# Kernel optimization log

Hardware: AMD Instinct MI355X
Metric: run time of the kernel (lower is better)

## Reference

```python
import jax, jax.numpy as jnp
import numpy as np
import math

MAXL = 3
TAUS = [16, 16, 16, 16]
OUT_TAUS = [16, 16, 16, 16]
BM_CNT = 1.0
BM_EPS = 1e-5

# (l1, l2, l) triples in the kernel's triple-loop order, bucketed by output l
TRIPLES = {l: [] for l in range(MAXL + 1)}
for _l1 in range(MAXL + 1):
    for _l2 in range(_l1 + 1):
        for _l in range(_l1 - _l2, min(_l1 + _l2, MAXL) + 1):
            TRIPLES[_l].append((_l1, _l2))

MIDDLE_TAUS = [sum(TAUS[a] * TAUS[b] for (a, b) in TRIPLES[l]) for l in range(MAXL + 1)]


def _cg_coef(l1, m1, l2, m2, l, m):
    if m1 + m2 != m:
        return 0.0
    f = math.factorial
    pre = math.sqrt((2 * l + 1) * f(l1 + l2 - l) * f(l1 - l2 + l) * f(-l1 + l2 + l) / f(l1 + l2 + l + 1))
    pre *= math.sqrt(f(l + m) * f(l - m) * f(l1 - m1) * f(l1 + m1) * f(l2 - m2) * f(l2 + m2))
    s = 0.0
    for k in range(0, l1 + l2 - l + 1):
        d = [k, l1 + l2 - l - k, l1 - m1 - k, l2 + m2 - k, l - l2 + m1 + k, l - l1 - m2 + k]
        if any(x < 0 for x in d):
            continue
        den = 1.0
        for x in d:
            den *= f(x)
        s += (-1.0) ** k / den
    return pre * s


def _cg_tensor(l1, l2, l):
    t = np.zeros((2 * l1 + 1, 2 * l2 + 1, 2 * l + 1), dtype=np.float32)
    for i, m1 in enumerate(range(-l1, l1 + 1)):
        for j, m2 in enumerate(range(-l2, l2 + 1)):
            m = m1 + m2
            if -l <= m <= l:
                t[i, j, m + l] = _cg_coef(l1, m1, l2, m2, l, m)
    return t

CG = {}
for _l in range(MAXL + 1):
    for (_l1, _l2) in TRIPLES[_l]:
        CG[(_l1, _l2, _l)] = jnp.asarray(_cg_tensor(_l1, _l2, _l))

# complex-multiply contraction tensor: (a*b)[k] = a[i] b[j] CM[i,j,k]
_CM = np.zeros((2, 2, 2), dtype=np.float32)
_CM[0, 0, 0] = 1.0; _CM[1, 1, 0] = -1.0; _CM[0, 1, 1] = 1.0; _CM[1, 0, 1] = 1.0
CM = jnp.asarray(_CM)


def setup_inputs() -> dict:
    key = jax.random.key(0)
    k1, k2, k3 = jax.random.split(key, 3)
    in_len = sum(TAUS[l] * (2 * l + 1) for l in range(MAXL + 1))  # 256
    wlen = sum(OUT_TAUS[l] * MIDDLE_TAUS[l] for l in range(MAXL + 1))  # 90112
    activations = jax.random.normal(k1, (2048, in_len, 2), dtype=jnp.float32)
    W = 0.05 * jax.random.uniform(k2, (wlen, 2), dtype=jnp.float32)
    bn_stds = jax.random.uniform(k3, (sum(MIDDLE_TAUS),), dtype=jnp.float32)
    return {"activations": activations, "W": W, "bn_stds": bn_stds}


def reference(activations, W, bn_stds):
    B = activations.shape[0]
    # split input into per-l parts: [B, tau_l, 2l+1, 2]
    Fs = []
    st = 0
    for l in range(MAXL + 1):
        ln = TAUS[l] * (2 * l + 1)
        Fs.append(activations[:, st:st + ln, :].reshape(B, TAUS[l], 2 * l + 1, 2))
        st += ln
    outs = []
    w_st = 0
    s_st = 0
    for l in range(MAXL + 1):
        # Clebsch-Gordan products feeding output degree l
        mids = []
        for (l1, l2) in TRIPLES[l]:
            c = jnp.einsum('btmi,bsnj,mnp,ijk->btspk', Fs[l1], Fs[l2], CG[(l1, l2, l)], CM)
            mids.append(c.reshape(B, TAUS[l1] * TAUS[l2], 2 * l + 1, 2))
        mid = jnp.concatenate(mids, axis=1)  # [B, M_l, 2l+1, 2]
        Ml = MIDDLE_TAUS[l]
        # fused batchnorm: per-middle-channel std over batch and m, moving average update
        batch_std = jnp.sqrt(jnp.mean(jnp.sum(mid * mid, axis=-1), axis=(0, 2)))  # [M_l]
        mov = bn_stds[s_st:s_st + Ml]
        new_std = (mov * BM_CNT + batch_std) / (BM_CNT + 1.0)
        mid = mid / (new_std + BM_EPS)[None, :, None, None]
        # complex linear mix over middle channels -> out_taus[l]
        wl = jax.lax.dynamic_slice_in_dim(W, w_st, OUT_TAUS[l] * Ml, axis=0).reshape(OUT_TAUS[l], Ml, 2)
        out_l = jnp.einsum('oci,bcmj,ijk->bomk', wl, mid, CM)
        outs.append(out_l.reshape(B, OUT_TAUS[l] * (2 * l + 1), 2))
        w_st += OUT_TAUS[l] * Ml
        s_st += Ml
    return jnp.concatenate(outs, axis=1)  # [B, 256, 2]
```

## Files before the change

kernel.cpp:

```cpp
#include <hip/hip_runtime.h>
#include <math.h>

typedef __attribute__((ext_vector_type(8))) short bf16x8;
typedef __attribute__((ext_vector_type(4))) float f32x4;

constexpr double cfact(int n){ double r=1.0; for(int i=2;i<=n;++i) r*=(double)i; return r; }
constexpr double csqrt_(double x){ double g=(x>1.0)?x:1.0; for(int i=0;i<100;++i) g=0.5*(g+x/g); return g; }
constexpr double cg_coef_(int l1,int m1,int l2,int m2,int l,int m){
  double pre = csqrt_((double)(2*l+1)*cfact(l1+l2-l)*cfact(l1-l2+l)*cfact(-l1+l2+l)/cfact(l1+l2+l+1));
  pre = pre*csqrt_(cfact(l+m)*cfact(l-m)*cfact(l1-m1)*cfact(l1+m1)*cfact(l2-m2)*cfact(l2+m2));
  double s=0.0;
  for(int k=0;k<=l1+l2-l;++k){
    int d0=k,d1=l1+l2-l-k,d2=l1-m1-k,d3=l2+m2-k,d4=l-l2+m1+k,d5=l-l1-m2+k;
    if(d0<0||d1<0||d2<0||d3<0||d4<0||d5<0) continue;
    double den=cfact(d0)*cfact(d1)*cfact(d2)*cfact(d3)*cfact(d4)*cfact(d5);
    s+=((k&1)?-1.0:1.0)/den;
  }
  return pre*s;
}
struct CGList{ int n; float coef[64]; int mi[64]; int ni[64]; int pi[64]; };
constexpr CGList build_cg(int l1,int l2,int l){
  CGList T{};
  for(int i=0;i<2*l1+1;++i){
    for(int j=0;j<2*l2+1;++j){
      int m1=i-l1, m2=j-l2, m=m1+m2;
      if(m<-l||m>l) continue;
      double c=cg_coef_(l1,m1,l2,m2,l,m);
      if(c>1e-12||c<-1e-12){
        T.coef[T.n]=(float)c; T.mi[T.n]=i; T.ni[T.n]=j; T.pi[T.n]=m+l; T.n++;
      }
    }
  }
  return T;
}

__device__ __host__ constexpr int AOFF(int l){ return l==0?0: l==1?16: l==2?64:144; }
__device__ __host__ constexpr int MLs(int l){ return l==0?1024: l==1?1536: l==2?1792:1536; }
__device__ __host__ constexpr int WOFF(int l){ return l==0?0: l==1?16384: l==2?40960:69632; }
__device__ __host__ constexpr int SOFF(int l){ return l==0?0: l==1?1024: l==2?2560:4352; }
__device__ __host__ constexpr int NTRI(int l){ return l==0?4: l==1?6: l==2?7:6; }
__device__ __host__ constexpr int ABASE(int l){ return l==0?0: l==1?65536: l==2?163840:278528; }
__device__ __host__ constexpr size_t MBW(int l){ return l==0?0 : l==1?2097152 : l==2?11534336 : 29884416; }
#define MID_OFF 1048576
#define MID_BYTES ((size_t)51904512*4)

#define DEVFN __device__ __forceinline__
#define LPITCH 144
#define APITCH 132

DEVFN unsigned f2bf2(float x, float y){
  unsigned ux = __float_as_uint(x); ux = (ux + 0x7FFFu + ((ux>>16)&1u)) >> 16;
  unsigned uy = __float_as_uint(y); uy = (uy + 0x7FFFu + ((uy>>16)&1u)) >> 16;
  return (ux & 0xFFFFu) | (uy << 16);
}

template<int L1,int L2,int L>
DEVFN void cg_accum(const float2* F1, const float2* F2, float2* mid){
  constexpr CGList T = build_cg(L1,L2,L);
  #pragma unroll
  for(int e=0;e<T.n;++e){
    const float c = T.coef[e];
    const float2 a = F1[T.mi[e]];
    const float2 b = F2[T.ni[e]];
    float pr = a.x*b.x - a.y*b.y;
    float pim= a.x*b.y + a.y*b.x;
    mid[T.pi[e]].x += c*pr;
    mid[T.pi[e]].y += c*pim;
  }
}

template<int L1,int L2,int L,int Q>
DEVFN void k1_body(const float2* __restrict__ acts, int b0, int u, int bh,
                   float& ssa, float& ssb, unsigned* __restrict__ midw){
  constexpr int N1=2*L1+1, N2=2*L2+1, NP=2*L+1, Ml=MLs(L);
  const int t = u>>3, s0 = (u&7)*2;
  unsigned* midq = midw ? (midw + MBW(L) + (size_t)Q*256) : nullptr;
  #pragma unroll 2
  for(int bi=0;bi<8;++bi){
    const int row = bh*8 + bi;
    const float2* arow = acts + row*256;
    float2 F1[N1], F2a[N2], F2b[N2], mida[NP], midb[NP];
    #pragma unroll
    for(int m=0;m<N1;++m) F1[m]=arow[AOFF(L1)+t*N1+m];
    #pragma unroll
    for(int n=0;n<N2;++n){
      F2a[n]=arow[AOFF(L2)+s0*N2+n];
      F2b[n]=arow[AOFF(L2)+(s0+1)*N2+n];
    }
    #pragma unroll
    for(int p=0;p<NP;++p){ mida[p]=make_float2(0.f,0.f); midb[p]=make_float2(0.f,0.f); }
    cg_accum<L1,L2,L>(F1,F2a,mida);
    cg_accum<L1,L2,L>(F1,F2b,midb);
    #pragma unroll
    for(int p=0;p<NP;++p){
      ssa += mida[p].x*mida[p].x + mida[p].y*mida[p].y;
      ssb += midb[p].x*midb[p].x + midb[p].y*midb[p].y;
    }
    if(midq){
      const size_t nrow = (size_t)(b0+row)*NP;
      #pragma unroll
      for(int p=0;p<NP;++p){
        uint2 v; v.x = f2bf2(mida[p].x, mida[p].y); v.y = f2bf2(midb[p].x, midb[p].y);
        ((uint2*)(midq + (nrow+p)*Ml))[u] = v;
      }
    }
  }
}

__global__ __launch_bounds__(256) void k_sumsq(const float* __restrict__ act,
                                               float* __restrict__ sumsq,
                                               unsigned* __restrict__ midw){
  __shared__ float2 acts[16*256];
  int bid=blockIdx.x;
  const int order[23] = {22,16,21,18,15,20,13,9,14,8,17,7,12,6,10,3,5,19,2,11,1,4,0};
  int ti = order[bid>>7];
  int b0 = (bid&127)*16;
  const int tid = threadIdx.x;
  {
    const float4* ag = (const float4*)act + (size_t)b0*128;
    float4* as4 = (float4*)acts;
    #pragma unroll
    for(int j=0;j<8;++j) as4[j*256+tid] = ag[j*256+tid];
  }
  __syncthreads();
  const int u = tid & 127, bh = tid >> 7;
  float ssa=0.f, ssb=0.f;
  switch(ti){
    case 0:  k1_body<0,0,0,0>(acts,b0,u,bh,ssa,ssb,midw); break;
    case 1:  k1_body<1,1,0,1>(acts,b0,u,bh,ssa,ssb,midw); break;
    case 2:  k1_body<2,2,0,2>(acts,b0,u,bh,ssa,ssb,midw); break;
    case 3:  k1_body<3,3,0,3>(acts,b0,u,bh,ssa,ssb,midw); break;
    case 4:  k1_body<1,0,1,0>(acts,b0,u,bh,ssa,ssb,midw); break;
    case 5:  k1_body<1,1,1,1>(acts,b0,u,bh,ssa,ssb,midw); break;
    case 6:  k1_body<2,1,1,2>(acts,b0,u,bh,ssa,ssb,midw); break;
    case 7:  k1_body<2,2,1,3>(acts,b0,u,bh,ssa,ssb,midw); break;
    case 8:  k1_body<3,2,1,4>(acts,b0,u,bh,ssa,ssb,midw); break;
    case 9:  k1_body<3,3,1,5>(acts,b0,u,bh,ssa,ssb,midw); break;
    case 10: k1_body<1,1,2,0>(acts,b0,u,bh,ssa,ssb,midw); break;
    case 11: k1_body<2,0,2,1>(acts,b0,u,bh,ssa,ssb,midw); break;
    case 12: k1_body<2,1,2,2>(acts,b0,u,bh,ssa,ssb,midw); break;
    case 13: k1_body<2,2,2,3>(acts,b0,u,bh,ssa,ssb,midw); break;
    case 14: k1_body<3,1,2,4>(acts,b0,u,bh,ssa,ssb,midw); break;
    case 15: k1_body<3,2,2,5>(acts,b0,u,bh,ssa,ssb,midw); break;
    case 16: k1_body<3,3,2,6>(acts,b0,u,bh,ssa,ssb,midw); break;
    case 17: k1_body<2,1,3,0>(acts,b0,u,bh,ssa,ssb,midw); break;
    case 18: k1_body<2,2,3,1>(acts,b0,u,bh,ssa,ssb,midw); break;
    case 19: k1_body<3,0,3,2>(acts,b0,u,bh,ssa,ssb,midw); break;
    case 20: k1_body<3,1,3,3>(acts,b0,u,bh,ssa,ssb,midw); break;
    case 21: k1_body<3,2,3,4>(acts,b0,u,bh,ssa,ssb,midw); break;
    default: k1_body<3,3,3,5>(acts,b0,u,bh,ssa,ssb,midw); break;
  }
  atomicAdd(&sumsq[ti*256 + 2*u],     ssa);
  atomicAdd(&sumsq[ti*256 + 2*u + 1], ssb);
}

__global__ __launch_bounds__(256) void k_buildA(const float* __restrict__ W,
                                                const float* __restrict__ bn,
                                                const float* __restrict__ sumsq,
                                                short* __restrict__ A){
  int idx = blockIdx.x*256 + threadIdx.x;
  if(idx>=5888) return;
  int l = (idx<1024)?0 : (idx<2560)?1 : (idx<4352)?2 : 3;
  float divi = (l==0)?(1.f/2048.f) : (l==1)?(1.f/6144.f) : (l==2)?(1.f/10240.f) : (1.f/14336.f);
  float bstd = sqrtf(sumsq[idx]*divi);
  float nstd = 0.5f*(bn[idx]+bstd);
  float s = 1.f/(nstd+1e-5f);
  int c = idx - SOFF(l);
  int Ml = MLs(l);
  const float2* wbase = (const float2*)W + WOFF(l) + c;
  unsigned* Aw = (unsigned*)(A + ABASE(l));
  for(int o=0;o<16;++o){
    float2 w = wbase[(size_t)o*Ml];
    Aw[(size_t)o*Ml + c]      = f2bf2(w.x*s, -w.y*s);
    Aw[(size_t)(o+16)*Ml + c] = f2bf2(w.y*s,  w.x*s);
  }
}

template<int L>
DEVFN void k4_panel(int tg, const unsigned* __restrict__ midl,
                    const short* __restrict__ A_l, float* __restrict__ out,
                    unsigned* ldsA){
  constexpr int NP = 2*L+1;
  constexpr int Ml = MLs(L);
  constexpr int NK = Ml/16;
  constexpr int P  = NK/8;
  const int tid = threadIdx.x;
  const int lane = tid & 63, w = tid >> 6;
  const int col = lane & 15, quad = lane >> 4;
  const int nt = tg*8 + w;
  const unsigned* Aw = (const unsigned*)A_l;
  const unsigned* bp = midl + (size_t)(nt*16 + col)*Ml + quad*4;

  const int r0 = tid >> 5,        j0 = (tid & 31)*4;
  const int r1 = (tid+512) >> 5,  j1 = j0;

  f32x4 cR = {0.f,0.f,0.f,0.f};
  f32x4 cI = {0.f,0.f,0.f,0.f};
  {
    uint4 v0 = *(const uint4*)(Aw + (size_t)r0*Ml + j0);
    uint4 v1 = *(const uint4*)(Aw + (size_t)r1*Ml + j1);
    *(uint4*)(ldsA + r0*APITCH + j0) = v0;
    *(uint4*)(ldsA + r1*APITCH + j1) = v1;
  }
  __syncthreads();
  for(int p=0; p<P; ++p){
    const unsigned* buf  = ldsA + (p&1)*(32*APITCH);
    unsigned* nbuf = ldsA + ((p+1)&1)*(32*APITCH);
    uint4 v0, v1;
    if(p+1 < P){
      v0 = *(const uint4*)(Aw + (size_t)r0*Ml + (p+1)*128 + j0);
      v1 = *(const uint4*)(Aw + (size_t)r1*Ml + (p+1)*128 + j1);
    }
    const unsigned* bpp = bp + p*128;
    const unsigned* a0 = buf + col*APITCH + quad*4;
    const unsigned* a1 = buf + (col+16)*APITCH + quad*4;
    #pragma unroll
    for(int c=0; c<8; ++c){
      bf16x8 b  = *(const bf16x8*)(bpp + c*16);
      bf16x8 A0 = *(const bf16x8*)(a0 + c*16);
      bf16x8 A1 = *(const bf16x8*)(a1 + c*16);
      cR = __builtin_amdgcn_mfma_f32_16x16x32_bf16(A0, b, cR, 0, 0, 0);
      cI = __builtin_amdgcn_mfma_f32_16x16x32_bf16(A1, b, cI, 0, 0, 0);
    }
    if(p+1 < P){
      *(uint4*)(nbuf + r0*APITCH + j0) = v0;
      *(uint4*)(nbuf + r1*APITCH + j1) = v1;
    }
    __syncthreads();
  }
  const int n = nt*16 + col;
  const int b = n / NP, pp = n % NP;
  float2* out2 = (float2*)out;
  #pragma unroll
  for(int i=0;i<4;++i){
    const int o = quad*4 + i;
    out2[(size_t)b*256 + AOFF(L) + o*NP + pp] = make_float2(cR[i], cI[i]);
  }
}

__global__ __launch_bounds__(512) void k_gemm4(const unsigned* __restrict__ midw,
                                               const short* __restrict__ A,
                                               float* __restrict__ out){
  __shared__ unsigned ldsA[2*32*APITCH];
  const int bid = blockIdx.x;
  if(bid < 16)       k4_panel<0>(bid,       midw+MBW(0), A+ABASE(0), out, ldsA);
  else if(bid < 64)  k4_panel<1>(bid - 16,  midw+MBW(1), A+ABASE(1), out, ldsA);
  else if(bid < 144) k4_panel<2>(bid - 64,  midw+MBW(2), A+ABASE(2), out, ldsA);
  else               k4_panel<3>(bid - 144, midw+MBW(3), A+ABASE(3), out, ldsA);
}

template<int L1,int L2,int L>
DEVFN void phase1(const float2* __restrict__ act2, unsigned* ldsw,
                  int half, int c0, int bh4, int b_lo, int b_hi, int n0){
  constexpr int N1=2*L1+1, N2=2*L2+1, NP=2*L+1;
  const int s  = c0 & 15;
  const int t1 = half*8 + (c0>>4);
  const int t2 = t1 + 4;
  for(int b = b_lo + bh4; b <= b_hi; b += 4){
    const float2* arow = act2 + (size_t)b*256;
    float2 F1a[N1], F1b[N1], F2[N2], mida[NP], midb[NP];
    #pragma unroll
    for(int m=0;m<N1;++m){
      F1a[m]=arow[AOFF(L1)+t1*N1+m];
      F1b[m]=arow[AOFF(L1)+t2*N1+m];
    }
    #pragma unroll
    for(int n=0;n<N2;++n) F2[n]=arow[AOFF(L2)+s*N2+n];
    #pragma unroll
    for(int p=0;p<NP;++p){ mida[p]=make_float2(0.f,0.f); midb[p]=make_float2(0.f,0.f); }
    cg_accum<L1,L2,L>(F1a,F2,mida);
    cg_accum<L1,L2,L>(F1b,F2,midb);
    int nb = b*NP - n0;
    #pragma unroll
    for(int p=0;p<NP;++p){
      int n = nb + p;
      if(n>=0 && n<32){
        ldsw[n*LPITCH + c0]      = f2bf2(mida[p].x, mida[p].y);
        ldsw[n*LPITCH + c0 + 64] = f2bf2(midb[p].x, midb[p].y);
      }
    }
  }
}

template<int L>
DEVFN void p1_dispatch(int q, int half, const float2* __restrict__ act2, unsigned* ldsw,
                       int c0,int bh4,int b_lo,int b_hi,int n0){
  if constexpr(L==0){
    switch(q){
      case 0: phase1<0,0,0>(act2,ldsw,half,c0,bh4,b_lo,b_hi,n0); break;
      case 1: phase1<1,1,0>(act2,ldsw,half,c0,bh4,b_lo,b_hi,n0); break;
      case 2: phase1<2,2,0>(act2,ldsw,half,c0,bh4,b_lo,b_hi,n0); break;
      default:phase1<3,3,0>(act2,ldsw,half,c0,bh4,b_lo,b_hi,n0); break;
    }
  } else if constexpr(L==1){
    switch(q){
      case 0: phase1<1,0,1>(act2,ldsw,half,c0,bh4,b_lo,b_hi,n0); break;
      case 1: phase1<1,1,1>(act2,ldsw,half,c0,bh4,b_lo,b_hi,n0); break;
      case 2: phase1<2,1,1>(act2,ldsw,half,c0,bh4,b_lo,b_hi,n0); break;
      case 3: phase1<2,2,1>(act2,ldsw,half,c0,bh4,b_lo,b_hi,n0); break;
      case 4: phase1<3,2,1>(act2,ldsw,half,c0,bh4,b_lo,b_hi,n0); break;
      default:phase1<3,3,1>(act2,ldsw,half,c0,bh4,b_lo,b_hi,n0); break;
    }
  } else if constexpr(L==2){
    switch(q){
      case 0: phase1<1,1,2>(act2,ldsw,half,c0,bh4,b_lo,b_hi,n0); break;
      case 1: phase1<2,0,2>(act2,ldsw,half,c0,bh4,b_lo,b_hi,n0); break;
      case 2: phase1<2,1,2>(act2,ldsw,half,c0,bh4,b_lo,b_hi,n0); break;
      case 3: phase1<2,2,2>(act2,ldsw,half,c0,bh4,b_lo,b_hi,n0); break;
      case 4: phase1<3,1,2>(act2,ldsw,half,c0,bh4,b_lo,b_hi,n0); break;
      case 5: phase1<3,2,2>(act2,ldsw,half,c0,bh4,b_lo,b_hi,n0); break;
      default:phase1<3,3,2>(act2,ldsw,half,c0,bh4,b_lo,b_hi,n0); break;
    }
  } else {
    switch(q){
      case 0: phase1<2,1,3>(act2,ldsw,half,c0,bh4,b_lo,b_hi,n0); break;
      case 1: phase1<2,2,3>(act2,ldsw,half,c0,bh4,b_lo,b_hi,n0); break;
      case 2: phase1<3,0,3>(act2,ldsw,half,c0,bh4,b_lo,b_hi,n0); break;
      case 3: phase1<3,1,3>(act2,ldsw,half,c0,bh4,b_lo,b_hi,n0); break;
      case 4: phase1<3,2,3>(act2,ldsw,half,c0,bh4,b_lo,b_hi,n0); break;
      default:phase1<3,3,3>(act2,ldsw,half,c0,bh4,b_lo,b_hi,n0); break;
    }
  }
}

template<int L>
DEVFN void k3_gemm(int n0, const float2* __restrict__ act2,
                   const short* __restrict__ A_l, float* __restrict__ out,
                   unsigned* lds){
  constexpr int NP = 2*L+1;
  constexpr int NT = NTRI(L);
  constexpr int pitchA = 2*MLs(L);
  const int tid = threadIdx.x;
  const int lane = tid & 63, wsub = tid >> 6;
  const int col = lane & 15, quad = lane >> 4;
  const int nh = wsub & 1, mh = wsub >> 1;
  const int c0 = tid & 63, bh4 = tid >> 6;
  const int b_lo = n0 / NP;
  const int b_hi = (n0 + 31) / NP;

  f32x4 acc = {0.f,0.f,0.f,0.f};
  const short* Ar = A_l + (size_t)(col + mh*16) * pitchA + quad*8;
  const int lds_rd = (nh*16 + col)*LPITCH + quad*4;

  for(int chunk = 0; chunk < 2*NT; ++chunk){
    const int q = chunk >> 1, half = chunk & 1;
    unsigned* buf = lds + (chunk & 1)*(32*LPITCH);
    p1_dispatch<L>(q, half, act2, buf, c0, bh4, b_lo, b_hi, n0);
    __syncthreads();
    const int kbase = q*512 + half*256;
    const char* ldsb = (const char*)(buf + lds_rd);
    #pragma unroll
    for(int ks=0; ks<8; ++ks){
      bf16x8 a = *(const bf16x8*)(Ar + kbase + ks*32);
      bf16x8 b = *(const bf16x8*)(ldsb + ks*64);
      acc = __builtin_amdgcn_mfma_f32_16x16x32_bf16(a, b, acc, 0, 0, 0);
    }
  }
  const int n = n0 + nh*16 + col;
  const int b = n / NP, p = n % NP;
  #pragma unroll
  for(int i=0;i<4;++i){
    const int o = quad*4 + i;
    out[((size_t)b*256 + AOFF(L) + o*NP + p)*2 + mh] = acc[i];
  }
}

__global__ __launch_bounds__(256) void k_gemm(const float* __restrict__ act,
                                              const short* __restrict__ A,
                                              float* __restrict__ out){
  __shared__ unsigned lds[2*32*LPITCH];
  const int bid = blockIdx.x;
  const float2* act2 = (const float2*)act;
  if(bid < 64)       k3_gemm<0>((bid      )*32, act2, A + ABASE(0), out, lds);
  else if(bid < 256) k3_gemm<1>((bid - 64 )*32, act2, A + ABASE(1), out, lds);
  else if(bid < 576) k3_gemm<2>((bid - 256)*32, act2, A + ABASE(2), out, lds);
  else               k3_gemm<3>((bid - 576)*32, act2, A + ABASE(3), out, lds);
}

extern "C" void kernel_launch(void* const* d_in, const int* in_sizes, int n_in,
                              void* d_out, int out_size, void* d_ws, size_t ws_size,
                              hipStream_t stream) {
  const float* act = (const float*)d_in[0];
  const float* W   = (const float*)d_in[1];
  const float* bn  = (const float*)d_in[2];
  float* out = (float*)d_out;

  float* sumsq = (float*)d_ws;
  short* A     = (short*)((char*)d_ws + 24576);
  const size_t REQ = (size_t)MID_OFF + MID_BYTES;
  unsigned* midw = (ws_size >= REQ) ? (unsigned*)((char*)d_ws + MID_OFF) : nullptr;

  hipMemsetAsync(sumsq, 0, 5888*sizeof(float), stream);
  hipLaunchKernelGGL(k_sumsq,  dim3(23*128), dim3(256), 0, stream, act, sumsq, midw);
  hipLaunchKernelGGL(k_buildA, dim3(23),     dim3(256), 0, stream, W, bn, sumsq, A);
  if(midw)
    hipLaunchKernelGGL(k_gemm4, dim3(256),  dim3(512), 0, stream, (const unsigned*)midw, A, out);
  else
    hipLaunchKernelGGL(k_gemm,  dim3(1024), dim3(256), 0, stream, act, A, out);
}
```

Baseline: 171.2 us.

## Fuse CG product recomputation into GEMM and drop materialized middle buffer

Before, k_sumsq wrote the full bf16 middle tensor to workspace and k_gemm4 streamed it back as GEMM operand. Now each block takes one (triple, 8-batch) tile, stages activations in LDS, recomputes the CG products into an LDS bf16 tile, runs the MFMA against the weight slice, and atomically adds partial outputs per triple into a zeroed output. This removes the large global write and reread of the middle tensor. The cost is recomputing the CG products, extra atomics, an output memset, and poor MFMA use for small-l tiles where many waves sit idle.

```diff
diff --git a/kernel.cpp b/kernel.cpp
--- a/kernel.cpp
+++ b/kernel.cpp
@@ -38,15 +38,10 @@
 __device__ __host__ constexpr int MLs(int l){ return l==0?1024: l==1?1536: l==2?1792:1536; }
 __device__ __host__ constexpr int WOFF(int l){ return l==0?0: l==1?16384: l==2?40960:69632; }
 __device__ __host__ constexpr int SOFF(int l){ return l==0?0: l==1?1024: l==2?2560:4352; }
-__device__ __host__ constexpr int NTRI(int l){ return l==0?4: l==1?6: l==2?7:6; }
 __device__ __host__ constexpr int ABASE(int l){ return l==0?0: l==1?65536: l==2?163840:278528; }
 __device__ __host__ constexpr size_t MBW(int l){ return l==0?0 : l==1?2097152 : l==2?11534336 : 29884416; }
-#define MID_OFF 1048576
-#define MID_BYTES ((size_t)51904512*4)
 
 #define DEVFN __device__ __forceinline__
-#define LPITCH 144
-#define APITCH 132
 
 DEVFN unsigned f2bf2(float x, float y){
   unsigned ux = __float_as_uint(x); ux = (ux + 0x7FFFu + ((ux>>16)&1u)) >> 16;
@@ -176,205 +171,124 @@
   }
 }
 
-template<int L>
-DEVFN void k4_panel(int tg, const unsigned* __restrict__ midl,
-                    const short* __restrict__ A_l, float* __restrict__ out,
-                    unsigned* ldsA){
-  constexpr int NP = 2*L+1;
+template<int L1,int L2,int L,int Q>
+DEVFN void kf_body(const float* __restrict__ act, const short* __restrict__ A_l,
+                   float* __restrict__ out, int b0, char* smem){
+  constexpr int N1=2*L1+1, N2=2*L2+1, NP=2*L+1;
   constexpr int Ml = MLs(L);
-  constexpr int NK = Ml/16;
-  constexpr int P  = NK/8;
+  constexpr int S1 = 16*N1;
+  constexpr int SH = (L1==L2)?0:S1;
+  constexpr int S12 = S1 + ((L1==L2)?0:16*N2);
+  constexpr int F4B = S12/2;
+  constexpr int ROWS = 8*NP;
+  constexpr int NTIL = (ROWS+15)/16;
+  constexpr int BP = 68;
   const int tid = threadIdx.x;
+  float2* sa = (float2*)smem;
+  unsigned* btile = (unsigned*)(smem + (size_t)8*S12*sizeof(float2));
+  {
+    const float4* actg = (const float4*)act;
+    float4* s4 = (float4*)smem;
+    for(int i=tid; i<8*F4B; i+=256){
+      int lb = i / F4B, e = i - lb*F4B;
+      int so = (e < S1/2) ? (AOFF(L1)/2 + e) : (AOFF(L2)/2 + (e - S1/2));
+      s4[i] = actg[(size_t)(b0+lb)*128 + so];
+    }
+  }
+  __syncthreads();
   const int lane = tid & 63, w = tid >> 6;
   const int col = lane & 15, quad = lane >> 4;
-  const int nt = tg*8 + w;
+  const int up = tid & 31, bi = tid >> 5;
   const unsigned* Aw = (const unsigned*)A_l;
-  const unsigned* bp = midl + (size_t)(nt*16 + col)*Ml + quad*4;
-
-  const int r0 = tid >> 5,        j0 = (tid & 31)*4;
-  const int r1 = (tid+512) >> 5,  j1 = j0;
-
   f32x4 cR = {0.f,0.f,0.f,0.f};
   f32x4 cI = {0.f,0.f,0.f,0.f};
-  {
-    uint4 v0 = *(const uint4*)(Aw + (size_t)r0*Ml + j0);
-    uint4 v1 = *(const uint4*)(Aw + (size_t)r1*Ml + j1);
-    *(uint4*)(ldsA + r0*APITCH + j0) = v0;
-    *(uint4*)(ldsA + r1*APITCH + j1) = v1;
-  }
-  __syncthreads();
-  for(int p=0; p<P; ++p){
-    const unsigned* buf  = ldsA + (p&1)*(32*APITCH);
-    unsigned* nbuf = ldsA + ((p+1)&1)*(32*APITCH);
-    uint4 v0, v1;
-    if(p+1 < P){
-      v0 = *(const uint4*)(Aw + (size_t)r0*Ml + (p+1)*128 + j0);
-      v1 = *(const uint4*)(Aw + (size_t)r1*Ml + (p+1)*128 + j1);
-    }
-    const unsigned* bpp = bp + p*128;
-    const unsigned* a0 = buf + col*APITCH + quad*4;
-    const unsigned* a1 = buf + (col+16)*APITCH + quad*4;
-    #pragma unroll
-    for(int c=0; c<8; ++c){
-      bf16x8 b  = *(const bf16x8*)(bpp + c*16);
-      bf16x8 A0 = *(const bf16x8*)(a0 + c*16);
-      bf16x8 A1 = *(const bf16x8*)(a1 + c*16);
-      cR = __builtin_amdgcn_mfma_f32_16x16x32_bf16(A0, b, cR, 0, 0, 0);
-      cI = __builtin_amdgcn_mfma_f32_16x16x32_bf16(A1, b, cI, 0, 0, 0);
-    }
-    if(p+1 < P){
-      *(uint4*)(nbuf + r0*APITCH + j0) = v0;
-      *(uint4*)(nbuf + r1*APITCH + j1) = v1;
+  #pragma unroll
+  for(int cc=0; cc<4; ++cc){
+    {
+      const int u = cc*32 + up;
+      const int t = u>>3, s0 = (u&7)*2;
+      const float2* f1b = sa + bi*S12 + t*N1;
+      const float2* f2b = sa + bi*S12 + SH;
+      float2 F1[N1], F2a[N2], F2b[N2], mida[NP], midb[NP];
+      #pragma unroll
+      for(int m=0;m<N1;++m) F1[m]=f1b[m];
+      #pragma unroll
+      for(int n=0;n<N2;++n){ F2a[n]=f2b[s0*N2+n]; F2b[n]=f2b[(s0+1)*N2+n]; }
+      #pragma unroll
+      for(int p=0;p<NP;++p){ mida[p]=make_float2(0.f,0.f); midb[p]=make_float2(0.f,0.f); }
+      cg_accum<L1,L2,L>(F1,F2a,mida);
+      cg_accum<L1,L2,L>(F1,F2b,midb);
+      unsigned* bw = btile + 2*up;
+      #pragma unroll
+      for(int p=0;p<NP;++p){
+        const int r = bi*NP + p;
+        bw[r*BP]   = f2bf2(mida[p].x, mida[p].y);
+        bw[r*BP+1] = f2bf2(midb[p].x, midb[p].y);
+      }
     }
     __syncthreads();
-  }
-  const int n = nt*16 + col;
-  const int b = n / NP, pp = n % NP;
-  float2* out2 = (float2*)out;
-  #pragma unroll
-  for(int i=0;i<4;++i){
-    const int o = quad*4 + i;
-    out2[(size_t)b*256 + AOFF(L) + o*NP + pp] = make_float2(cR[i], cI[i]);
-  }
-}
-
-__global__ __launch_bounds__(512) void k_gemm4(const unsigned* __restrict__ midw,
+    if(w < NTIL){
+      const unsigned* Ab = Aw + Q*256 + cc*64 + quad*4;
+      const unsigned* bb = btile + (w*16+col)*BP + quad*4;
+      #pragma unroll
+      for(int ks=0; ks<4; ++ks){
+        bf16x8 A0 = *(const bf16x8*)(Ab + (size_t)col*Ml + ks*16);
+        bf16x8 A1 = *(const bf16x8*)(Ab + (size_t)(col+16)*Ml + ks*16);
+        bf16x8 b  = *(const bf16x8*)(bb + ks*16);
+        cR = __builtin_amdgcn_mfma_f32_16x16x32_bf16(A0, b, cR, 0, 0, 0);
+        cI = __builtin_amdgcn_mfma_f32_16x16x32_bf16(A1, b, cI, 0, 0, 0);
+      }
+    }
+    __syncthreads();
+  }
+  if(w < NTIL){
+    const int r = w*16 + col;
+    if(r < ROWS){
+      const int b = b0 + r/NP, p = r - (r/NP)*NP;
+      float* ob = out + ((size_t)b*256 + AOFF(L) + p)*2;
+      #pragma unroll
+      for(int i=0;i<4;++i){
+        const int o = quad*4 + i;
+        atomicAdd(ob + o*NP*2,     cR[i]);
+        atomicAdd(ob + o*NP*2 + 1, cI[i]);
+      }
+    }
+  }
+}
+
+__global__ __launch_bounds__(256) void k_fused(const float* __restrict__ act,
                                                const short* __restrict__ A,
                                                float* __restrict__ out){
-  __shared__ unsigned ldsA[2*32*APITCH];
+  __shared__ __align__(16) char smem[29696];
   const int bid = blockIdx.x;
-  if(bid < 16)       k4_panel<0>(bid,       midw+MBW(0), A+ABASE(0), out, ldsA);
-  else if(bid < 64)  k4_panel<1>(bid - 16,  midw+MBW(1), A+ABASE(1), out, ldsA);
-  else if(bid < 144) k4_panel<2>(bid - 64,  midw+MBW(2), A+ABASE(2), out, ldsA);
-  else               k4_panel<3>(bid - 144, midw+MBW(3), A+ABASE(3), out, ldsA);
-}
-
-template<int L1,int L2,int L>
-DEVFN void phase1(const float2* __restrict__ act2, unsigned* ldsw,
-                  int half, int c0, int bh4, int b_lo, int b_hi, int n0){
-  constexpr int N1=2*L1+1, N2=2*L2+1, NP=2*L+1;
-  const int s  = c0 & 15;
-  const int t1 = half*8 + (c0>>4);
-  const int t2 = t1 + 4;
-  for(int b = b_lo + bh4; b <= b_hi; b += 4){
-    const float2* arow = act2 + (size_t)b*256;
-    float2 F1a[N1], F1b[N1], F2[N2], mida[NP], midb[NP];
-    #pragma unroll
-    for(int m=0;m<N1;++m){
-      F1a[m]=arow[AOFF(L1)+t1*N1+m];
-      F1b[m]=arow[AOFF(L1)+t2*N1+m];
-    }
-    #pragma unroll
-    for(int n=0;n<N2;++n) F2[n]=arow[AOFF(L2)+s*N2+n];
-    #pragma unroll
-    for(int p=0;p<NP;++p){ mida[p]=make_float2(0.f,0.f); midb[p]=make_float2(0.f,0.f); }
-    cg_accum<L1,L2,L>(F1a,F2,mida);
-    cg_accum<L1,L2,L>(F1b,F2,midb);
-    int nb = b*NP - n0;
-    #pragma unroll
-    for(int p=0;p<NP;++p){
-      int n = nb + p;
-      if(n>=0 && n<32){
-        ldsw[n*LPITCH + c0]      = f2bf2(mida[p].x, mida[p].y);
-        ldsw[n*LPITCH + c0 + 64] = f2bf2(midb[p].x, midb[p].y);
-      }
-    }
-  }
-}
-
-template<int L>
-DEVFN void p1_dispatch(int q, int half, const float2* __restrict__ act2, unsigned* ldsw,
-                       int c0,int bh4,int b_lo,int b_hi,int n0){
-  if constexpr(L==0){
-    switch(q){
-      case 0: phase1<0,0,0>(act2,ldsw,half,c0,bh4,b_lo,b_hi,n0); break;
-      case 1: phase1<1,1,0>(act2,ldsw,half,c0,bh4,b_lo,b_hi,n0); break;
-      case 2: phase1<2,2,0>(act2,ldsw,half,c0,bh4,b_lo,b_hi,n0); break;
-      default:phase1<3,3,0>(act2,ldsw,half,c0,bh4,b_lo,b_hi,n0); break;
-    }
-  } else if constexpr(L==1){
-    switch(q){
-      case 0: phase1<1,0,1>(act2,ldsw,half,c0,bh4,b_lo,b_hi,n0); break;
-      case 1: phase1<1,1,1>(act2,ldsw,half,c0,bh4,b_lo,b_hi,n0); break;
-      case 2: phase1<2,1,1>(act2,ldsw,half,c0,bh4,b_lo,b_hi,n0); break;
-      case 3: phase1<2,2,1>(act2,ldsw,half,c0,bh4,b_lo,b_hi,n0); break;
-      case 4: phase1<3,2,1>(act2,ldsw,half,c0,bh4,b_lo,b_hi,n0); break;
-      default:phase1<3,3,1>(act2,ldsw,half,c0,bh4,b_lo,b_hi,n0); break;
-    }
-  } else if constexpr(L==2){
-    switch(q){
-      case 0: phase1<1,1,2>(act2,ldsw,half,c0,bh4,b_lo,b_hi,n0); break;
-      case 1: phase1<2,0,2>(act2,ldsw,half,c0,bh4,b_lo,b_hi,n0); break;
-      case 2: phase1<2,1,2>(act2,ldsw,half,c0,bh4,b_lo,b_hi,n0); break;
-      case 3: phase1<2,2,2>(act2,ldsw,half,c0,bh4,b_lo,b_hi,n0); break;
-      case 4: phase1<3,1,2>(act2,ldsw,half,c0,bh4,b_lo,b_hi,n0); break;
-      case 5: phase1<3,2,2>(act2,ldsw,half,c0,bh4,b_lo,b_hi,n0); break;
-      default:phase1<3,3,2>(act2,ldsw,half,c0,bh4,b_lo,b_hi,n0); break;
-    }
-  } else {
-    switch(q){
-      case 0: phase1<2,1,3>(act2,ldsw,half,c0,bh4,b_lo,b_hi,n0); break;
-      case 1: phase1<2,2,3>(act2,ldsw,half,c0,bh4,b_lo,b_hi,n0); break;
-      case 2: phase1<3,0,3>(act2,ldsw,half,c0,bh4,b_lo,b_hi,n0); break;
-      case 3: phase1<3,1,3>(act2,ldsw,half,c0,bh4,b_lo,b_hi,n0); break;
-      case 4: phase1<3,2,3>(act2,ldsw,half,c0,bh4,b_lo,b_hi,n0); break;
-      default:phase1<3,3,3>(act2,ldsw,half,c0,bh4,b_lo,b_hi,n0); break;
-    }
-  }
-}
-
-template<int L>
-DEVFN void k3_gemm(int n0, const float2* __restrict__ act2,
-                   const short* __restrict__ A_l, float* __restrict__ out,
-                   unsigned* lds){
-  constexpr int NP = 2*L+1;
-  constexpr int NT = NTRI(L);
-  constexpr int pitchA = 2*MLs(L);
-  const int tid = threadIdx.x;
-  const int lane = tid & 63, wsub = tid >> 6;
-  const int col = lane & 15, quad = lane >> 4;
-  const int nh = wsub & 1, mh = wsub >> 1;
-  const int c0 = tid & 63, bh4 = tid >> 6;
-  const int b_lo = n0 / NP;
-  const int b_hi = (n0 + 31) / NP;
-
-  f32x4 acc = {0.f,0.f,0.f,0.f};
-  const short* Ar = A_l + (size_t)(col + mh*16) * pitchA + quad*8;
-  const int lds_rd = (nh*16 + col)*LPITCH + quad*4;
-
-  for(int chunk = 0; chunk < 2*NT; ++chunk){
-    const int q = chunk >> 1, half = chunk & 1;
-    unsigned* buf = lds + (chunk & 1)*(32*LPITCH);
-    p1_dispatch<L>(q, half, act2, buf, c0, bh4, b_lo, b_hi, n0);
-    __syncthreads();
-    const int kbase = q*512 + half*256;
-    const char* ldsb = (const char*)(buf + lds_rd);
-    #pragma unroll
-    for(int ks=0; ks<8; ++ks){
-      bf16x8 a = *(const bf16x8*)(Ar + kbase + ks*32);
-      bf16x8 b = *(const bf16x8*)(ldsb + ks*64);
-      acc = __builtin_amdgcn_mfma_f32_16x16x32_bf16(a, b, acc, 0, 0, 0);
-    }
-  }
-  const int n = n0 + nh*16 + col;
-  const int b = n / NP, p = n % NP;
-  #pragma unroll
-  for(int i=0;i<4;++i){
-    const int o = quad*4 + i;
-    out[((size_t)b*256 + AOFF(L) + o*NP + p)*2 + mh] = acc[i];
-  }
-}
-
-__global__ __launch_bounds__(256) void k_gemm(const float* __restrict__ act,
-                                              const short* __restrict__ A,
-                                              float* __restrict__ out){
-  __shared__ unsigned lds[2*32*LPITCH];
-  const int bid = blockIdx.x;
-  const float2* act2 = (const float2*)act;
-  if(bid < 64)       k3_gemm<0>((bid      )*32, act2, A + ABASE(0), out, lds);
-  else if(bid < 256) k3_gemm<1>((bid - 64 )*32, act2, A + ABASE(1), out, lds);
-  else if(bid < 576) k3_gemm<2>((bid - 256)*32, act2, A + ABASE(2), out, lds);
-  else               k3_gemm<3>((bid - 576)*32, act2, A + ABASE(3), out, lds);
+  const int order[23] = {22,16,21,18,15,20,13,9,14,8,17,7,12,6,10,3,5,19,2,11,1,4,0};
+  const int ti = order[bid>>8];
+  const int b0 = (bid&255)*8;
+  switch(ti){
+    case 0:  kf_body<0,0,0,0>(act, A+ABASE(0), out, b0, smem); break;
+    case 1:  kf_body<1,1,0,1>(act, A+ABASE(0), out, b0, smem); break;
+    case 2:  kf_body<2,2,0,2>(act, A+ABASE(0), out, b0, smem); break;
+    case 3:  kf_body<3,3,0,3>(act, A+ABASE(0), out, b0, smem); break;
+    case 4:  kf_body<1,0,1,0>(act, A+ABASE(1), out, b0, smem); break;
+    case 5:  kf_body<1,1,1,1>(act, A+ABASE(1), out, b0, smem); break;
+    case 6:  kf_body<2,1,1,2>(act, A+ABASE(1), out, b0, smem); break;
+    case 7:  kf_body<2,2,1,3>(act, A+ABASE(1), out, b0, smem); break;
+    case 8:  kf_body<3,2,1,4>(act, A+ABASE(1), out, b0, smem); break;
+    case 9:  kf_body<3,3,1,5>(act, A+ABASE(1), out, b0, smem); break;
+    case 10: kf_body<1,1,2,0>(act, A+ABASE(2), out, b0, smem); break;
+    case 11: kf_body<2,0,2,1>(act, A+ABASE(2), out, b0, smem); break;
+    case 12: kf_body<2,1,2,2>(act, A+ABASE(2), out, b0, smem); break;
+    case 13: kf_body<2,2,2,3>(act, A+ABASE(2), out, b0, smem); break;
+    case 14: kf_body<3,1,2,4>(act, A+ABASE(2), out, b0, smem); break;
+    case 15: kf_body<3,2,2,5>(act, A+ABASE(2), out, b0, smem); break;
+    case 16: kf_body<3,3,2,6>(act, A+ABASE(2), out, b0, smem); break;
+    case 17: kf_body<2,1,3,0>(act, A+ABASE(3), out, b0, smem); break;
+    case 18: kf_body<2,2,3,1>(act, A+ABASE(3), out, b0, smem); break;
+    case 19: kf_body<3,0,3,2>(act, A+ABASE(3), out, b0, smem); break;
+    case 20: kf_body<3,1,3,3>(act, A+ABASE(3), out, b0, smem); break;
+    case 21: kf_body<3,2,3,4>(act, A+ABASE(3), out, b0, smem); break;
+    default: kf_body<3,3,3,5>(act, A+ABASE(3), out, b0, smem); break;
+  }
 }
 
 extern "C" void kernel_launch(void* const* d_in, const int* in_sizes, int n_in,
@@ -387,14 +301,10 @@
 
   float* sumsq = (float*)d_ws;
   short* A     = (short*)((char*)d_ws + 24576);
-  const size_t REQ = (size_t)MID_OFF + MID_BYTES;
-  unsigned* midw = (ws_size >= REQ) ? (unsigned*)((char*)d_ws + MID_OFF) : nullptr;
 
   hipMemsetAsync(sumsq, 0, 5888*sizeof(float), stream);
-  hipLaunchKernelGGL(k_sumsq,  dim3(23*128), dim3(256), 0, stream, act, sumsq, midw);
+  hipMemsetAsync(out, 0, (size_t)2048*256*2*sizeof(float), stream);
+  hipLaunchKernelGGL(k_sumsq,  dim3(23*128), dim3(256), 0, stream, act, sumsq, (unsigned*)nullptr);
   hipLaunchKernelGGL(k_buildA, dim3(23),     dim3(256), 0, stream, W, bn, sumsq, A);
-  if(midw)
-    hipLaunchKernelGGL(k_gemm4, dim3(256),  dim3(512), 0, stream, (const unsigned*)midw, A, out);
-  else
-    hipLaunchKernelGGL(k_gemm,  dim3(1024), dim3(256), 0, stream, act, A, out);
-}
+  hipLaunchKernelGGL(k_fused,  dim3(23*256), dim3(256), 0, stream, act, A, out);
+}
```

New measurement: 251.3 us. +46.8%, slower.
